# Optimization experiments

Measured on AMD Instinct MI355X. Metric: run time of the kernel, lower is better.

## Reference

```python
import jax, jax.numpy as jnp
import numpy as np

NUM_CLUSTERS = 64
CLUSTER_DIM = 256
TOKEN_DIM = 256
MLP_DIM = 512
THRESHOLD = 0.7
EPS = 1e-12  # torch F.normalize eps


def setup_inputs() -> dict:
    key = jax.random.key(0)
    ks = jax.random.split(key, 6)
    B, N, D = 64, 256, 768
    s = lambda fan: 1.0 / np.sqrt(fan)
    return {
        "local_features": jax.random.normal(ks[0], (B, N, D), jnp.float32),
        "global_token": jax.random.normal(ks[1], (B, D), jnp.float32),
        "W1_local": jax.random.normal(ks[2], (D, MLP_DIM), jnp.float32) * s(D),
        "b1_local": jnp.zeros((MLP_DIM,), jnp.float32),
        "W2_local": jax.random.normal(ks[3], (MLP_DIM, NUM_CLUSTERS * CLUSTER_DIM), jnp.float32) * s(MLP_DIM),
        "b2_local": jnp.zeros((NUM_CLUSTERS * CLUSTER_DIM,), jnp.float32),
        "W1_global": jax.random.normal(ks[4], (D, MLP_DIM), jnp.float32) * s(D),
        "b1_global": jnp.zeros((MLP_DIM,), jnp.float32),
        "W2_global": jax.random.normal(ks[5], (MLP_DIM, TOKEN_DIM), jnp.float32) * s(MLP_DIM),
        "b2_global": jnp.zeros((TOKEN_DIM,), jnp.float32),
        "k_nearest": 10,
    }


def _extract_features(local_features, global_token,
                      W1_local, b1_local, W2_local, b2_local,
                      W1_global, b1_global, W2_global, b2_global):
    B = local_features.shape[0]
    # mlp_local: Linear -> ReLU -> Linear
    h = jax.nn.relu(local_features @ W1_local + b1_local)          # [B, N, mlp]
    local = (h @ W2_local + b2_local).reshape(B, -1, NUM_CLUSTERS, CLUSTER_DIM)  # [B, N, K, C]
    # NetVLAD-style: softmax over patch axis, then sum over patches
    local = jax.nn.softmax(local, axis=1).sum(axis=1)              # [B, K, C]
    local = local.reshape(B, NUM_CLUSTERS * CLUSTER_DIM)           # [B, K*C]
    # mlp_global
    g = jax.nn.relu(global_token @ W1_global + b1_global) @ W2_global + b2_global  # [B, token_dim]
    feats = jnp.concatenate([local, g], axis=1)                    # [B, out_dim]
    norm = jnp.maximum(jnp.linalg.norm(feats, axis=1, keepdims=True), EPS)
    return feats / norm


def _covisibility(features, k_nearest):
    N = features.shape[0]
    sim = features @ features.T                                    # [N, N]
    mask = (sim > THRESHOLD).astype(jnp.float32)
    k = min(int(k_nearest), N)
    if k > 0:
        _, idx = jax.lax.top_k(sim, k)                             # [N, k]
        rows = jnp.broadcast_to(jnp.arange(N)[:, None], idx.shape)
        mask = mask.at[rows, idx].set(1.0)                         # mask[i, idx[i]] = 1
        mask = mask.at[idx, rows].set(1.0)                         # mask[idx[i], i] = 1
    diag = jnp.arange(N)
    mask = mask.at[diag, diag].set(1.0)
    return mask


def reference(local_features, global_token,
              W1_local, b1_local, W2_local, b2_local,
              W1_global, b1_global, W2_global, b2_global,
              k_nearest):
    feats = _extract_features(local_features, global_token,
                              W1_local, b1_local, W2_local, b2_local,
                              W1_global, b1_global, W2_global, b2_global)
    mask = _covisibility(feats, k_nearest)
    return feats, mask
```

## Files before the change

kernel.cpp:

```cpp
#include <hip/hip_runtime.h>
#include <math.h>

#define TOKDIM   256
#define DD       768
#define HDIM     512
#define LOCALDIM 16384
#define FEATDIM  16640
#define BB       64
#define THRESH   0.7f
#define ONEF     0x3f800000u
#define GP       65


__global__ __launch_bounds__(1024) void k1_mlp(
    const float* __restrict__ gtok, const float* __restrict__ W1,
    const float* __restrict__ b1,   const float* __restrict__ W2,
    float* __restrict__ pg,         unsigned* __restrict__ maskU)
{
    __shared__ float  xs[DD];
    __shared__ float4 hh4[32][32];
    __shared__ float  hs[128];
    __shared__ float4 gg4[16][64];
    const int blk = blockIdx.x, t = threadIdx.x;
    const int b = blk >> 2, uc = blk & 3;

    if (blk == 0) {
        maskU[t] = 0u; maskU[t + 1024] = 0u; maskU[t + 2048] = 0u; maskU[t + 3072] = 0u;
    }
    if (t < DD) xs[t] = gtok[b * DD + t];
    __syncthreads();

    {
        const int u4 = t & 31, q = t >> 5;
        const float4* w = (const float4*)W1 + (size_t)(q * 24) * 128 + uc * 32 + u4;
        float4 a = make_float4(0.f, 0.f, 0.f, 0.f);
        #pragma unroll 8
        for (int d = 0; d < 24; ++d) {
            const float x = xs[q * 24 + d];
            const float4 wv = w[(size_t)d * 128];
            a.x = fmaf(x, wv.x, a.x); a.y = fmaf(x, wv.y, a.y);
            a.z = fmaf(x, wv.z, a.z); a.w = fmaf(x, wv.w, a.w);
        }
        hh4[q][u4] = a;
    }
    __syncthreads();
    if (t < 128) {
        const float* h = (const float*)hh4;
        float s = b1[uc * 128 + t];
        #pragma unroll
        for (int q = 0; q < 32; ++q) s += h[q * 128 + t];
        hs[t] = fmaxf(s, 0.f);
    }
    __syncthreads();

    {
        const int o4 = t & 63, jq = t >> 6;
        const float4* w = (const float4*)W2 + (size_t)(uc * 128 + jq * 8) * 64 + o4;
        float4 a = make_float4(0.f, 0.f, 0.f, 0.f);
        #pragma unroll
        for (int j = 0; j < 8; ++j) {
            const float hv = hs[jq * 8 + j];
            const float4 wv = w[(size_t)j * 64];
            a.x = fmaf(hv, wv.x, a.x); a.y = fmaf(hv, wv.y, a.y);
            a.z = fmaf(hv, wv.z, a.z); a.w = fmaf(hv, wv.w, a.w);
        }
        gg4[jq][o4] = a;
    }
    __syncthreads();
    if (t < 256) {
        const float* g = (const float*)gg4;
        float s = 0.f;
        #pragma unroll
        for (int q = 0; q < 16; ++q) s += g[q * 256 + t];
        pg[((size_t)uc * BB + b) * TOKDIM + t] = s;
    }
}

__global__ __launch_bounds__(1024) void k2_simmask(
    const float* __restrict__ pg, const float* __restrict__ b2,
    const int* __restrict__ kptr, float* __restrict__ feats,
    unsigned* __restrict__ maskU)
{
    __shared__ float gT[TOKDIM][GP];
    __shared__ float part[16][BB];
    __shared__ float invs[BB];
    const int i = blockIdx.x, t = threadIdx.x;

    #pragma unroll
    for (int it = 0; it < 16; ++it) {
        const int idx = it * 1024 + t;
        const int j = idx >> 8, d = idx & 255;
        const float v = b2[d]
            + pg[((size_t)0 * BB + j) * TOKDIM + d]
            + pg[((size_t)1 * BB + j) * TOKDIM + d]
            + pg[((size_t)2 * BB + j) * TOKDIM + d]
            + pg[((size_t)3 * BB + j) * TOKDIM + d];
        gT[d][j] = v;
    }
    __syncthreads();

    {
        const int q = t >> 6, j = t & 63;
        float s = 0.f;
        #pragma unroll
        for (int dd = 0; dd < 16; ++dd) { const float v = gT[q * 16 + dd][j]; s = fmaf(v, v, s); }
        part[q][j] = s;
    }
    __syncthreads();
    if (t < BB) {
        float ssq = 0.f;
        #pragma unroll
        for (int q = 0; q < 16; ++q) ssq += part[q][t];
        invs[t] = 1.f / fmaxf(sqrtf((float)LOCALDIM + ssq), 1e-12f);
    }
    __syncthreads();
    const float inv = invs[i];

    {
        float4* f4 = (float4*)(feats + (size_t)i * FEATDIM);
        const float4 v = make_float4(inv, inv, inv, inv);
        f4[t] = v; f4[t + 1024] = v; f4[t + 2048] = v; f4[t + 3072] = v;
        if (t < TOKDIM) feats[(size_t)i * FEATDIM + LOCALDIM + t] = gT[t][i] * inv;
    }

    {
        const int q = t >> 6, j = t & 63;
        float s = 0.f;
        #pragma unroll
        for (int dd = 0; dd < 16; ++dd)
            s = fmaf(gT[q * 16 + dd][i], gT[q * 16 + dd][j], s);
        part[q][j] = s;
    }
    __syncthreads();
    if (t < BB) {
        float dot = 0.f;
        #pragma unroll
        for (int q = 0; q < 16; ++q) dot += part[q][t];
        const float sv = ((float)LOCALDIM + dot) * inv * invs[t];
        int k = *kptr; if (k > BB) k = BB;
        float v = sv;
        unsigned long long rowbits = 0;
        for (int p = 0; p < k; ++p) {
            float m = v;
            #pragma unroll
            for (int off = 32; off > 0; off >>= 1) m = fmaxf(m, __shfl_xor(m, off));
            const unsigned long long ball = __ballot(v == m);
            const int bi = __ffsll(ball) - 1;
            rowbits |= 1ull << bi;
            if (t == bi) v = -INFINITY;
            if (t == 0) atomicOr(&maskU[bi * BB + i], ONEF);
        }
        const unsigned base =
            ((sv > THRESH) || (t == i) || ((rowbits >> t) & 1ull)) ? ONEF : 0u;
        if (base) atomicOr(&maskU[i * BB + t], base);
    }
}

extern "C" void kernel_launch(void* const* d_in, const int* in_sizes, int n_in,
                              void* d_out, int out_size, void* d_ws, size_t ws_size,
                              hipStream_t stream) {
    const float* gtok = (const float*)d_in[1];
    const float* W1g  = (const float*)d_in[6];
    const float* b1g  = (const float*)d_in[7];
    const float* W2g  = (const float*)d_in[8];
    const float* b2g  = (const float*)d_in[9];
    const int*   kp   = (const int*)d_in[10];

    float*    feats = (float*)d_out;
    unsigned* maskU = (unsigned*)(feats + (size_t)BB * FEATDIM);
    float*    pg    = (float*)d_ws;

    hipLaunchKernelGGL(k1_mlp,     dim3(256), dim3(1024), 0, stream,
                       gtok, W1g, b1g, W2g, pg, maskU);
    hipLaunchKernelGGL(k2_simmask, dim3(BB),  dim3(1024), 0, stream,
                       pg, b2g, kp, feats, maskU);
}
```

Measured before the change: 20.37 us.

## Process two batch rows per block and split hidden units eightfold in MLP kernel

The global MLP kernel now gives each block two batch rows and 64 hidden units instead of one row and 128 units. Each weight load is reused for two rows, which halves total W1/W2 traffic across the grid. Partial sums are reduced through padded shared buffers in two stages. The second kernel now sums eight partial slices with float4 loads and adds a barrier before reusing the shared partial array, which fixes a race. The cost is more partial-sum traffic through the workspace and extra shared-memory reduction passes.

```diff
diff --git a/kernel.cpp b/kernel.cpp
--- a/kernel.cpp
+++ b/kernel.cpp
@@ -1,101 +1,129 @@
 #include <hip/hip_runtime.h>
 #include <math.h>
 
-#define TOKDIM   256
 #define DD       768
 #define HDIM     512
+#define TOKDIM   256
 #define LOCALDIM 16384
 #define FEATDIM  16640
 #define BB       64
 #define THRESH   0.7f
 #define ONEF     0x3f800000u
-#define GP       65
-
-
-__global__ __launch_bounds__(1024) void k1_mlp(
+#define UC       8
+#define UNITS    64
+#define BPG      2
+
+
+__global__ __launch_bounds__(1024) void kA(
     const float* __restrict__ gtok, const float* __restrict__ W1,
     const float* __restrict__ b1,   const float* __restrict__ W2,
     float* __restrict__ pg,         unsigned* __restrict__ maskU)
 {
-    __shared__ float  xs[DD];
-    __shared__ float4 hh4[32][32];
-    __shared__ float  hs[128];
-    __shared__ float4 gg4[16][64];
+    __shared__ float  xs[BPG][DD];
+    __shared__ float4 buf[2112];
+    __shared__ float  pr[1024];
+    __shared__ float  hs[BPG][UNITS];
     const int blk = blockIdx.x, t = threadIdx.x;
-    const int b = blk >> 2, uc = blk & 3;
+    const int bg = blk >> 3, uc = blk & 7;
+    const int b0 = bg * BPG, u0 = uc * UNITS;
 
     if (blk == 0) {
-        maskU[t] = 0u; maskU[t + 1024] = 0u; maskU[t + 2048] = 0u; maskU[t + 3072] = 0u;
-    }
-    if (t < DD) xs[t] = gtok[b * DD + t];
-    __syncthreads();
-
-    {
-        const int u4 = t & 31, q = t >> 5;
-        const float4* w = (const float4*)W1 + (size_t)(q * 24) * 128 + uc * 32 + u4;
-        float4 a = make_float4(0.f, 0.f, 0.f, 0.f);
-        #pragma unroll 8
-        for (int d = 0; d < 24; ++d) {
-            const float x = xs[q * 24 + d];
+        maskU[t] = 0u; maskU[t+1024] = 0u; maskU[t+2048] = 0u; maskU[t+3072] = 0u;
+    }
+    for (int i = t; i < BPG * DD; i += 1024)
+        xs[i / DD][i % DD] = gtok[(size_t)(b0 + i / DD) * DD + (i % DD)];
+    __syncthreads();
+
+    {
+        const int u4 = t & 15, q = t >> 4, d0 = q * 12;
+        const float4* w = (const float4*)W1 + (size_t)d0 * 128 + uc * 16 + u4;
+        float4 a0 = {0,0,0,0}, a1 = {0,0,0,0};
+        #pragma unroll
+        for (int d = 0; d < 12; ++d) {
             const float4 wv = w[(size_t)d * 128];
-            a.x = fmaf(x, wv.x, a.x); a.y = fmaf(x, wv.y, a.y);
-            a.z = fmaf(x, wv.z, a.z); a.w = fmaf(x, wv.w, a.w);
-        }
-        hh4[q][u4] = a;
+            const float x0 = xs[0][d0+d], x1 = xs[1][d0+d];
+            a0.x = fmaf(x0, wv.x, a0.x); a0.y = fmaf(x0, wv.y, a0.y);
+            a0.z = fmaf(x0, wv.z, a0.z); a0.w = fmaf(x0, wv.w, a0.w);
+            a1.x = fmaf(x1, wv.x, a1.x); a1.y = fmaf(x1, wv.y, a1.y);
+            a1.z = fmaf(x1, wv.z, a1.z); a1.w = fmaf(x1, wv.w, a1.w);
+        }
+        buf[q * 33 + u4 * 2 + 0] = a0;
+        buf[q * 33 + u4 * 2 + 1] = a1;
+    }
+    __syncthreads();
+    {
+        const float* hf = (const float*)buf;
+        const int c = t & 127, qg = t >> 7;
+        float s = 0.f;
+        #pragma unroll
+        for (int qq = 0; qq < 8; ++qq) s += hf[(size_t)(qg*8+qq)*132 + c];
+        pr[qg * 128 + c] = s;
     }
     __syncthreads();
     if (t < 128) {
-        const float* h = (const float*)hh4;
-        float s = b1[uc * 128 + t];
-        #pragma unroll
-        for (int q = 0; q < 32; ++q) s += h[q * 128 + t];
-        hs[t] = fmaxf(s, 0.f);
+        const int u = ((t >> 3) << 2) | (t & 3), bb = (t >> 2) & 1;
+        float s = b1[u0 + u];
+        #pragma unroll
+        for (int qg = 0; qg < 8; ++qg) s += pr[qg * 128 + t];
+        hs[bb][u] = fmaxf(s, 0.f);
     }
     __syncthreads();
 
     {
         const int o4 = t & 63, jq = t >> 6;
-        const float4* w = (const float4*)W2 + (size_t)(uc * 128 + jq * 8) * 64 + o4;
-        float4 a = make_float4(0.f, 0.f, 0.f, 0.f);
-        #pragma unroll
-        for (int j = 0; j < 8; ++j) {
-            const float hv = hs[jq * 8 + j];
-            const float4 wv = w[(size_t)j * 64];
-            a.x = fmaf(hv, wv.x, a.x); a.y = fmaf(hv, wv.y, a.y);
-            a.z = fmaf(hv, wv.z, a.z); a.w = fmaf(hv, wv.w, a.w);
-        }
-        gg4[jq][o4] = a;
-    }
-    __syncthreads();
-    if (t < 256) {
-        const float* g = (const float*)gg4;
-        float s = 0.f;
-        #pragma unroll
-        for (int q = 0; q < 16; ++q) s += g[q * 256 + t];
-        pg[((size_t)uc * BB + b) * TOKDIM + t] = s;
+        const float4* w = (const float4*)W2 + (size_t)(u0 + jq * 4) * 64 + o4;
+        float4 a0 = {0,0,0,0}, a1 = {0,0,0,0};
+        #pragma unroll
+        for (int jj = 0; jj < 4; ++jj) {
+            const float4 wv = w[(size_t)jj * 64];
+            const float h0 = hs[0][jq*4+jj], h1 = hs[1][jq*4+jj];
+            a0.x = fmaf(h0, wv.x, a0.x); a0.y = fmaf(h0, wv.y, a0.y);
+            a0.z = fmaf(h0, wv.z, a0.z); a0.w = fmaf(h0, wv.w, a0.w);
+            a1.x = fmaf(h1, wv.x, a1.x); a1.y = fmaf(h1, wv.y, a1.y);
+            a1.z = fmaf(h1, wv.z, a1.z); a1.w = fmaf(h1, wv.w, a1.w);
+        }
+        buf[jq * 129 + o4 * 2 + 0] = a0;
+        buf[jq * 129 + o4 * 2 + 1] = a1;
+    }
+    __syncthreads();
+    {
+        const float* gf = (const float*)buf;
+        const int c = t & 511, qg = t >> 9;
+        float s = 0.f;
+        #pragma unroll
+        for (int qq = 0; qq < 8; ++qq) s += gf[(size_t)(qg*8+qq)*516 + c];
+        pr[qg * 512 + c] = s;
+    }
+    __syncthreads();
+    if (t < 512) {
+        const int o = ((t >> 3) << 2) | (t & 3), bb = (t >> 2) & 1;
+        pg[((size_t)uc * BB + b0 + bb) * TOKDIM + o] = pr[t] + pr[512 + t];
     }
 }
 
-__global__ __launch_bounds__(1024) void k2_simmask(
+__global__ __launch_bounds__(1024) void kB(
     const float* __restrict__ pg, const float* __restrict__ b2,
     const int* __restrict__ kptr, float* __restrict__ feats,
     unsigned* __restrict__ maskU)
 {
-    __shared__ float gT[TOKDIM][GP];
+    __shared__ float gT[TOKDIM][BB + 1];
     __shared__ float part[16][BB];
     __shared__ float invs[BB];
     const int i = blockIdx.x, t = threadIdx.x;
+    const float4* pg4 = (const float4*)pg;
+    const float4* b24 = (const float4*)b2;
 
     #pragma unroll
-    for (int it = 0; it < 16; ++it) {
-        const int idx = it * 1024 + t;
-        const int j = idx >> 8, d = idx & 255;
-        const float v = b2[d]
-            + pg[((size_t)0 * BB + j) * TOKDIM + d]
-            + pg[((size_t)1 * BB + j) * TOKDIM + d]
-            + pg[((size_t)2 * BB + j) * TOKDIM + d]
-            + pg[((size_t)3 * BB + j) * TOKDIM + d];
-        gT[d][j] = v;
+    for (int r = 0; r < 4; ++r) {
+        const int f = r * 1024 + t, j = f >> 6, d4 = f & 63;
+        float4 v = b24[d4];
+        #pragma unroll
+        for (int u = 0; u < UC; ++u) {
+            const float4 p = pg4[(size_t)u * 4096 + f];
+            v.x += p.x; v.y += p.y; v.z += p.z; v.w += p.w;
+        }
+        gT[d4*4+0][j] = v.x; gT[d4*4+1][j] = v.y;
+        gT[d4*4+2][j] = v.z; gT[d4*4+3][j] = v.w;
     }
     __syncthreads();
 
@@ -103,7 +131,7 @@
         const int q = t >> 6, j = t & 63;
         float s = 0.f;
         #pragma unroll
-        for (int dd = 0; dd < 16; ++dd) { const float v = gT[q * 16 + dd][j]; s = fmaf(v, v, s); }
+        for (int dd = 0; dd < 16; ++dd) { const float v = gT[q*16+dd][j]; s = fmaf(v, v, s); }
         part[q][j] = s;
     }
     __syncthreads();
@@ -122,13 +150,14 @@
         f4[t] = v; f4[t + 1024] = v; f4[t + 2048] = v; f4[t + 3072] = v;
         if (t < TOKDIM) feats[(size_t)i * FEATDIM + LOCALDIM + t] = gT[t][i] * inv;
     }
+    __syncthreads();
 
     {
         const int q = t >> 6, j = t & 63;
         float s = 0.f;
         #pragma unroll
         for (int dd = 0; dd < 16; ++dd)
-            s = fmaf(gT[q * 16 + dd][i], gT[q * 16 + dd][j], s);
+            s = fmaf(gT[q*16+dd][i], gT[q*16+dd][j], s);
         part[q][j] = s;
     }
     __syncthreads();
@@ -170,8 +199,8 @@
     unsigned* maskU = (unsigned*)(feats + (size_t)BB * FEATDIM);
     float*    pg    = (float*)d_ws;
 
-    hipLaunchKernelGGL(k1_mlp,     dim3(256), dim3(1024), 0, stream,
+    hipLaunchKernelGGL(kA, dim3(256), dim3(1024), 0, stream,
                        gtok, W1g, b1g, W2g, pg, maskU);
-    hipLaunchKernelGGL(k2_simmask, dim3(BB),  dim3(1024), 0, stream,
+    hipLaunchKernelGGL(kB, dim3(BB),  dim3(1024), 0, stream,
                        pg, b2g, kp, feats, maskU);
 }
```

After: 21.55 us. 1.06x slower.
